# Optimization experiments

Measured on AMD Instinct MI355X. Metric: run time of the kernel, lower is better.

The kernel has to match this reference:

```python
import jax, jax.numpy as jnp
import numpy as np
from jax import lax

EPS = 1e-12

V, D, L, B = 50000, 128, 2048, 64
K1, K2 = 64, 64
W1, W2, W3 = 8, 8, 8


def conv1d_same(x, w):
    # x: [B, L, Cin], w: [W, Cin, Cout] -> [B, L, Cout]
    return lax.conv_general_dilated(x, w, window_strides=(1,), padding='SAME',
                                    dimension_numbers=('NWC', 'WIO', 'NWC'))


def gru_final_state(x, Wx, Wh, b):
    # Keras GRU (reset_after=True, gate order z, r, h); returns final hidden state.
    # x: [B, L, D] -> h_T: [B, K2]
    U = Wh.shape[0]
    x_proj = jnp.einsum('bld,dk->blk', x, Wx) + b[0]  # [B, L, 3U]

    def step(h, xp_t):
        hp = h @ Wh + b[1]                       # [B, 3U]
        xz, xr, xh = jnp.split(xp_t, 3, axis=-1)
        hz, hr, hh_ = jnp.split(hp, 3, axis=-1)
        z = jax.nn.sigmoid(xz + hz)
        r = jax.nn.sigmoid(xr + hr)
        hh = jnp.tanh(xh + r * hh_)
        h_new = z * h + (1.0 - z) * hh
        return h_new, None

    h0 = jnp.zeros((x.shape[0], U), dtype=x.dtype)
    h_T, _ = lax.scan(step, h0, jnp.swapaxes(x_proj, 0, 1))
    return h_T


def setup_inputs() -> dict:
    key = jax.random.key(0)
    ks = jax.random.split(key, 10)
    s = 0.05
    return {
        'code_block': jax.random.randint(ks[0], (B, L), 0, V, dtype=jnp.int32),
        'E': jax.random.normal(ks[1], (V, D), jnp.float32) * s,
        'bias_table': jax.random.normal(ks[2], (V, 1), jnp.float32) * s,
        'Wx': jax.random.normal(ks[3], (D, 3 * K2), jnp.float32) * s,
        'Wh': jax.random.normal(ks[4], (K2, 3 * K2), jnp.float32) * s,
        'b_gru': jnp.zeros((2, 3 * K2), jnp.float32),
        'c1w': jax.random.normal(ks[5], (W1, D, K1), jnp.float32) * s,
        'c1b': jnp.zeros((K1,), jnp.float32),
        'c2w': jax.random.normal(ks[6], (W2, K1, K2), jnp.float32) * s,
        'c2b': jnp.zeros((K2,), jnp.float32),
        'c3w': jax.random.normal(ks[7], (W3, K2, 1), jnp.float32) * s,
        'c3b': jnp.zeros((1,), jnp.float32),
    }


def reference(code_block, E, bias_table, Wx, Wh, b_gru, c1w, c1b, c2w, c2b, c3w, c3b):
    tok = E[code_block]                          # [B, L, D] embedding gather
    bias = bias_table[code_block][..., 0]        # [B, L] per-token bias

    h_t = gru_final_state(tok, Wx, Wh, b_gru)    # [B, K2]

    # AttentionFeatures: conv -> relu -> conv -> * h_t -> l2-normalize (dropout off)
    L1 = jax.nn.relu(conv1d_same(tok, c1w) + c1b)        # [B, L, K1]
    L2 = (conv1d_same(L1, c2w) + c2b) * h_t[:, None, :]  # [B, L, K2]
    L_feat = L2 * lax.rsqrt(jnp.sum(L2 * L2, axis=-1, keepdims=True) + EPS)

    # AttentionWeights: conv to 1 channel, softmax over time
    a_logits = conv1d_same(L_feat, c3w)[..., 0] + c3b    # [B, L]
    alpha = jax.nn.softmax(a_logits, axis=-1)            # [B, L]

    # n_hat = sum_l alpha_l * embed_l
    n_hat = jnp.einsum('bl,bld->bd', alpha, tok)         # [B, D]

    # logits_l = <embed_l, n_hat> + bias_l ; softmax over positions
    logits = jnp.einsum('bld,bd->bl', tok, n_hat) + bias # [B, L]
    return jax.nn.softmax(logits, axis=-1)
```

## Files before the change

### kernel.cpp

```cpp
#include <hip/hip_runtime.h>

#define B_ 64
#define L_ 2048
#define D_ 128
#define LP 2056
#define PAD 3

typedef __attribute__((ext_vector_type(8))) short short8;
typedef __attribute__((ext_vector_type(4))) float f32x4;
typedef __attribute__((ext_vector_type(4))) unsigned short us4;

static __device__ __forceinline__ float bf2f(unsigned short u) {
  return __uint_as_float(((unsigned int)u) << 16);
}
static __device__ __forceinline__ unsigned short f2bf(float f) {
  unsigned int x = __float_as_uint(f);
  unsigned int r = (x + 0x7fffu + ((x >> 16) & 1u)) >> 16;
  return (unsigned short)r;
}

__global__ __launch_bounds__(256) void k_prep(
    const int* __restrict__ code, const float* __restrict__ E,
    const float* __restrict__ bias_table, const float* __restrict__ Wx,
    const float* __restrict__ c1w, const float* __restrict__ c2w,
    unsigned short* __restrict__ tokpad,
    unsigned short* __restrict__ WxT, unsigned short* __restrict__ c1wT,
    unsigned short* __restrict__ c2wT, float* __restrict__ biasg)
{
  int id = blockIdx.x * 256 + threadIdx.x;
  const int N0 = B_ * LP * 16;
  if (id < N0) {
    int b = id / (LP * 16); int rem = id % (LP * 16);
    int row = rem >> 4, c8 = rem & 15;
    uint4 o = {0u,0u,0u,0u};
    if (row >= PAD && row < PAD + L_) {
      int cd = code[b * L_ + (row - PAD)];
      const float4* e = (const float4*)(E + (size_t)cd * D_ + c8 * 8);
      float4 e0 = e[0], e1 = e[1];
      o.x = f2bf(e0.x) | ((unsigned int)f2bf(e0.y) << 16);
      o.y = f2bf(e0.z) | ((unsigned int)f2bf(e0.w) << 16);
      o.z = f2bf(e1.x) | ((unsigned int)f2bf(e1.y) << 16);
      o.w = f2bf(e1.z) | ((unsigned int)f2bf(e1.w) << 16);
    }
    ((uint4*)tokpad)[id] = o;
    return;
  }
  id -= N0;
  const int N2 = B_ * L_;
  if (id < N2) { biasg[id] = bias_table[code[id]]; return; }
  id -= N2;
  const int N3 = 192 * 128;
  if (id < N3) { int c = id >> 7, d = id & 127; WxT[id] = f2bf(Wx[d * 192 + c]); return; }
  id -= N3;
  const int N4 = 8 * 64 * 128;
  if (id < N4) {
    int w = id >> 13, c = (id >> 7) & 63, d = id & 127;
    c1wT[id] = f2bf(c1w[(w * 128 + d) * 64 + c]); return;
  }
  id -= N4;
  const int N5 = 8 * 64 * 64;
  if (id < N5) {
    int w = id >> 12, c = (id >> 6) & 63, d = id & 63;
    c2wT[id] = f2bf(c2w[(w * 64 + d) * 64 + c]);
  }
}

__global__ __launch_bounds__(256) void k_xproj(
    const unsigned short* __restrict__ tokpad, const unsigned short* __restrict__ WxT,
    const float* __restrict__ bg, unsigned short* __restrict__ xg)
{
  __shared__ __align__(16) unsigned short At[128 * 136];
  __shared__ __align__(16) unsigned short Bt[192 * 136];
  int b = blockIdx.x >> 4;
  int l0 = (blockIdx.x & 15) << 7;
  int tid = threadIdx.x;
  for (int i = tid; i < 128 * 16; i += 256) {
    int row = i >> 4, c8 = i & 15;
    uint4 v = ((const uint4*)tokpad)[(b * LP + PAD + l0 + row) * 16 + c8];
    *((uint4*)&At[row * 136 + c8 * 8]) = v;
  }
  for (int i = tid; i < 192 * 16; i += 256) {
    int row = i >> 4, c8 = i & 15;
    uint4 v = ((const uint4*)WxT)[i];
    *((uint4*)&Bt[row * 136 + c8 * 8]) = v;
  }
  __syncthreads();
  int wave = tid >> 6, lane = tid & 63;
  int m = lane & 15, q = lane >> 4;
  f32x4 acc[2][12];
  #pragma unroll
  for (int mt = 0; mt < 2; ++mt)
    #pragma unroll
    for (int nt = 0; nt < 12; ++nt) acc[mt][nt] = (f32x4){0.f,0.f,0.f,0.f};
  #pragma unroll
  for (int ks = 0; ks < 4; ++ks) {
    int kof = ks * 32 + q * 8;
    short8 a[2], bb[12];
    #pragma unroll
    for (int mt = 0; mt < 2; ++mt)
      a[mt] = *(const short8*)&At[(wave * 32 + mt * 16 + m) * 136 + kof];
    #pragma unroll
    for (int nt = 0; nt < 12; ++nt)
      bb[nt] = *(const short8*)&Bt[(nt * 16 + m) * 136 + kof];
    #pragma unroll
    for (int mt = 0; mt < 2; ++mt)
      #pragma unroll
      for (int nt = 0; nt < 12; ++nt)
        acc[mt][nt] = __builtin_amdgcn_mfma_f32_16x16x32_bf16(a[mt], bb[nt], acc[mt][nt], 0, 0, 0);
  }
  __syncthreads();
  #pragma unroll
  for (int mt = 0; mt < 2; ++mt) {
    int lrow = wave * 32 + mt * 16 + q * 4;
    #pragma unroll
    for (int nt = 0; nt < 12; ++nt) {
      int c = nt * 16 + m;
      float b0 = bg[c];
      us4 val;
      val.x = f2bf(acc[mt][nt][0] + b0);
      val.y = f2bf(acc[mt][nt][1] + b0);
      val.z = f2bf(acc[mt][nt][2] + b0);
      val.w = f2bf(acc[mt][nt][3] + b0);
      *((us4*)&Bt[c * 136 + lrow]) = val;
    }
  }
  __syncthreads();
  for (int i = tid; i < 64 * 32; i += 256) {
    int j = i >> 5, g = i & 31;
    us4 z4 = *(const us4*)&Bt[j * 136 + g * 4];
    us4 r4 = *(const us4*)&Bt[(64 + j) * 136 + g * 4];
    us4 h4 = *(const us4*)&Bt[(128 + j) * 136 + g * 4];
    uint4 o0, o1;
    o0.x = (unsigned)z4.x | ((unsigned)r4.x << 16); o0.y = (unsigned)h4.x;
    o0.z = (unsigned)z4.y | ((unsigned)r4.y << 16); o0.w = (unsigned)h4.y;
    o1.x = (unsigned)z4.z | ((unsigned)r4.z << 16); o1.y = (unsigned)h4.z;
    o1.z = (unsigned)z4.w | ((unsigned)r4.w << 16); o1.w = (unsigned)h4.w;
    size_t stp = (size_t)(b * 64 + j) * L_ + l0 + g * 4;
    ((uint4*)xg)[stp >> 1]       = o0;
    ((uint4*)xg)[(stp >> 1) + 1] = o1;
  }
}

#define BARRIER() asm volatile("s_waitcnt lgkmcnt(0)\n\ts_barrier" ::: "memory")

__global__ __launch_bounds__(192)
__attribute__((amdgpu_waves_per_eu(1, 1)))
void k_fused(
    const unsigned short* __restrict__ xg, const float* __restrict__ Wh,
    const float* __restrict__ bg, float* __restrict__ h_t,
    const unsigned short* __restrict__ tokpad,
    const unsigned short* __restrict__ c1wT, const float* __restrict__ c1b,
    const unsigned short* __restrict__ c2wT, const float* __restrict__ c2b,
    unsigned short* __restrict__ c2o)
{
  __shared__ __align__(16) unsigned short pool[39744];
  int bid = blockIdx.x;
  int tid = threadIdx.x;

  if (bid < 64) {
    int w = tid >> 6, j = tid & 63;
    float* xch = (float*)pool;
    int b = bid;
    int kb = w * 22;

    float wz[22], wr[22], wh[22];
    #pragma unroll
    for (int i = 0; i < 22; ++i) {
      int k = kb + i;
      bool ok = k < 64;
      wz[i] = ok ? Wh[k * 192 + j]       : 0.f;
      wr[i] = ok ? Wh[k * 192 + 64 + j]  : 0.f;
      wh[i] = ok ? Wh[k * 192 + 128 + j] : 0.f;
    }
    #pragma unroll
    for (int i = 0; i < 22; ++i)
      asm volatile("" : "+v"(wz[i]), "+v"(wr[i]), "+v"(wh[i]));

    float seedz = (w == 0) ? bg[192 + j]       : 0.f;
    float seedr = (w == 0) ? bg[192 + 64 + j]  : 0.f;
    float seedh = (w == 0) ? bg[192 + 128 + j] : 0.f;
    float hreg = 0.f;

    const uint4* xp = (const uint4*)(xg + (size_t)(b * 64 + j) * L_ * 4);
    uint4 cur_ = xp[0];
    uint4 nxt_ = xp[1];

#define STEP(WZR, WH_, P) { \
    float hk[22]; \
    _Pragma("unroll") \
    for (int i = 0; i < 22; ++i) \
      hk[i] = __int_as_float(__builtin_amdgcn_readlane(__float_as_int(hreg), (kb + i) & 63)); \
    __builtin_amdgcn_sched_barrier(0); \
    float az[4] = {seedz, 0.f, 0.f, 0.f}; \
    float ar[4] = {seedr, 0.f, 0.f, 0.f}; \
    float ah[4] = {seedh, 0.f, 0.f, 0.f}; \
    _Pragma("unroll") \
    for (int i = 0; i < 22; ++i) { \
      az[i & 3] = fmaf(hk[i], wz[i], az[i & 3]); \
      ar[i & 3] = fmaf(hk[i], wr[i], ar[i & 3]); \
      ah[i & 3] = fmaf(hk[i], wh[i], ah[i & 3]); \
    } \
    float4 pv; \
    pv.x = (az[0] + az[1]) + (az[2] + az[3]); \
    pv.y = (ar[0] + ar[1]) + (ar[2] + ar[3]); \
    pv.z = (ah[0] + ah[1]) + (ah[2] + ah[3]); \
    pv.w = 0.f; \
    *((float4*)&xch[(P) * 768 + (w * 64 + j) * 4]) = pv; \
    BARRIER(); \
    float4 q0 = *((const float4*)&xch[(P) * 768 + (0 * 64 + j) * 4]); \
    float4 q1 = *((const float4*)&xch[(P) * 768 + (1 * 64 + j) * 4]); \
    float4 q2 = *((const float4*)&xch[(P) * 768 + (2 * 64 + j) * 4]); \
    float sz = (q0.x + q1.x) + q2.x; \
    float sr = (q0.y + q1.y) + q2.y; \
    float sh = (q0.z + q1.z) + q2.z; \
    float xvz = bf2f((unsigned short)((WZR) & 0xffffu)); \
    float xvr = bf2f((unsigned short)((WZR) >> 16)); \
    float xvh = bf2f((unsigned short)((WH_) & 0xffffu)); \
    float zg = 1.f / (1.f + __expf(-(xvz + sz))); \
    float rg = 1.f / (1.f + __expf(-(xvr + sr))); \
    float e2 = __expf(-2.f * (xvh + rg * sh)); \
    float hh = fmaf(2.f, __frcp_rn(1.f + e2), -1.f); \
    hreg = zg * hreg + (1.f - zg) * hh; \
  }

    #pragma nounroll
    for (int p = 0; p < L_ / 2; ++p) {
      int pn = (p < L_ / 2 - 2) ? p + 2 : (L_ / 2 - 1);
      uint4 nn = xp[pn];
      STEP(cur_.x, cur_.y, 0)
      STEP(cur_.z, cur_.w, 1)
      cur_ = nxt_; nxt_ = nn;
    }
#undef STEP
    if (w == 0) h_t[b * 64 + j] = hreg;
    return;
  }

  unsigned short* At    = pool;
  unsigned short* l1buf = pool + 20672;
  unsigned short* Bw    = pool + 31040;
  int wv = tid >> 6, lane = tid & 63;
  int m = lane & 15, q = lane >> 4;

  for (int job = bid - 64; job < 1024; job += 192) {
    int b = job >> 4;
    int l0 = (job & 15) << 7;
    __syncthreads();
    for (int i = tid; i < 152 * 16; i += 192) {
      int row = i >> 4, c8 = i & 15;
      int p = l0 - 3 + row;
      p = p < 0 ? 0 : (p > 2055 ? 2055 : p);
      *((uint4*)&At[row * 136 + c8 * 8]) = ((const uint4*)tokpad)[(b * LP + p) * 16 + c8];
    }
    f32x4 acc[3][4];
    #pragma unroll
    for (int mt = 0; mt < 3; ++mt)
      #pragma unroll
      for (int nt = 0; nt < 4; ++nt) acc[mt][nt] = (f32x4){0.f,0.f,0.f,0.f};
    for (int w8 = 0; w8 < 8; ++w8) {
      __syncthreads();
      for (int i = tid; i < 64 * 16; i += 192) {
        int row = i >> 4, c8 = i & 15;
        *((uint4*)&Bw[row * 136 + c8 * 8]) = ((const uint4*)c1wT)[(w8 * 64 + row) * 16 + c8];
      }
      __syncthreads();
      #pragma unroll
      for (int ks = 0; ks < 4; ++ks) {
        int kof = ks * 32 + q * 8;
        short8 a[3], bb[4];
        #pragma unroll
        for (int mt = 0; mt < 3; ++mt) {
          int tl = wv + 3 * mt;
          a[mt] = *(const short8*)&At[(tl * 16 + m + w8) * 136 + kof];
        }
        #pragma unroll
        for (int nt = 0; nt < 4; ++nt)
          bb[nt] = *(const short8*)&Bw[(nt * 16 + m) * 136 + kof];
        #pragma unroll
        for (int mt = 0; mt < 3; ++mt)
          #pragma unroll
          for (int nt = 0; nt < 4; ++nt)
            acc[mt][nt] = __builtin_amdgcn_mfma_f32_16x16x32_bf16(a[mt], bb[nt], acc[mt][nt], 0, 0, 0);
      }
    }
    #pragma unroll
    for (int mt = 0; mt < 3; ++mt) {
      int tl = wv + 3 * mt;
      #pragma unroll
      for (int nt = 0; nt < 4; ++nt) {
        int c = nt * 16 + m;
        float bs = c1b[c];
        #pragma unroll
        for (int r = 0; r < 4; ++r) {
          float v = fmaxf(acc[mt][nt][r] + bs, 0.f);
          l1buf[(tl * 16 + q * 4 + r) * 72 + c] = f2bf(v);
        }
      }
    }
    __syncthreads();
    for (int i2 = tid; i2 < 135 * 8; i2 += 192) {
      int i = i2 >> 3, c8 = i2 & 7;
      int jrow = l0 - 3 + i;
      if (jrow < 0 || jrow > 2047) {
        uint4 z4 = {0u,0u,0u,0u};
        *((uint4*)&l1buf[i * 72 + c8 * 8]) = z4;
      }
    }
    f32x4 acc2[3][4];
    #pragma unroll
    for (int mt = 0; mt < 3; ++mt)
      #pragma unroll
      for (int nt = 0; nt < 4; ++nt) acc2[mt][nt] = (f32x4){0.f,0.f,0.f,0.f};
    for (int w8 = 0; w8 < 8; ++w8) {
      __syncthreads();
      for (int i = tid; i < 64 * 8; i += 192) {
        int row = i >> 3, c8 = i & 7;
        *((uint4*)&Bw[row * 72 + c8 * 8]) = ((const uint4*)c2wT)[(w8 * 64 + row) * 8 + c8];
      }
      __syncthreads();
      #pragma unroll
      for (int ks = 0; ks < 2; ++ks) {
        int kof = ks * 32 + q * 8;
        short8 a[3], bb[4];
        #pragma unroll
        for (int mt = 0; mt < 3; ++mt) {
          int tl = wv + 3 * mt;
          if (tl < 8)
            a[mt] = *(const short8*)&l1buf[(tl * 16 + m + w8) * 72 + kof];
        }
        #pragma unroll
        for (int nt = 0; nt < 4; ++nt)
          bb[nt] = *(const short8*)&Bw[(nt * 16 + m) * 72 + kof];
        #pragma unroll
        for (int mt = 0; mt < 3; ++mt) {
          int tl = wv + 3 * mt;
          if (tl < 8)
            #pragma unroll
            for (int nt = 0; nt < 4; ++nt)
              acc2[mt][nt] = __builtin_amdgcn_mfma_f32_16x16x32_bf16(a[mt], bb[nt], acc2[mt][nt], 0, 0, 0);
        }
      }
    }
    #pragma unroll
    for (int mt = 0; mt < 3; ++mt) {
      int tl = wv + 3 * mt;
      if (tl < 8) {
        #pragma unroll
        for (int nt = 0; nt < 4; ++nt) {
          int c = nt * 16 + m;
          float bs = c2b[c];
          #pragma unroll
          for (int r = 0; r < 4; ++r)
            c2o[(size_t)(b * L_ + l0 + tl * 16 + q * 4 + r) * 64 + c] = f2bf(acc2[mt][nt][r] + bs);
        }
      }
    }
  }
}

__global__ __launch_bounds__(256) void k_alpha(
    const unsigned short* __restrict__ c2o, const float* __restrict__ h_t,
    const float* __restrict__ c3w, const float* __restrict__ c3b,
    float* __restrict__ a_out)
{
  __shared__ float Lf[71 * 65];
  __shared__ float red[256];
  __shared__ float ht[64];
  __shared__ float c3[512];
  int b = blockIdx.x >> 5;
  int tile = blockIdx.x & 31;
  int tid = threadIdx.x, lane = tid & 63, wave = tid >> 6;
  if (tid < 64) ht[tid] = h_t[b * 64 + tid];
  for (int i = tid; i < 512; i += 256) c3[i] = c3w[i];
  float c3bias = c3b[0];
  __syncthreads();
  int lt = tile << 6;
  for (int i0 = wave; i0 < 71; i0 += 4) {
    int l = lt - 3 + i0;
    float v = 0.f;
    if (l >= 0 && l < L_) v = bf2f(c2o[((size_t)b * L_ + l) * 64 + lane]) * ht[lane];
    float ss = v * v;
    #pragma unroll
    for (int msk = 1; msk < 64; msk <<= 1) ss += __shfl_xor(ss, msk);
    Lf[i0 * 65 + lane] = v * rsqrtf(ss + 1e-12f);
  }
  __syncthreads();
  {
    int u = lane, part = wave;
    float p = 0.f;
    #pragma unroll
    for (int w = 0; w < 8; ++w)
      #pragma unroll
      for (int cc = 0; cc < 16; ++cc) {
        int c = part * 16 + cc;
        p += Lf[(u + w) * 65 + c] * c3[w * 64 + c];
      }
    red[tid] = p;
  }
  __syncthreads();
  if (tid < 64)
    a_out[b * L_ + lt + tid] = red[tid] + red[64 + tid] + red[128 + tid] + red[192 + tid] + c3bias;
}

__global__ __launch_bounds__(256) void k_fin(
    const unsigned short* __restrict__ tokpad, const float* __restrict__ a_in,
    const float* __restrict__ biasg, float* __restrict__ out)
{
  __shared__ float a_lds[2048];
  __shared__ float l_lds[2048];
  __shared__ float red[256];
  __shared__ float nred[512];
  __shared__ float nhat[128];
  int b = blockIdx.x, tid = threadIdx.x, lane = tid & 63, wave = tid >> 6;
  for (int i = tid; i < 2048; i += 256) a_lds[i] = a_in[b * L_ + i];
  __syncthreads();
  {
    float mx = -1e30f;
    for (int i = tid; i < 2048; i += 256) mx = fmaxf(mx, a_lds[i]);
    #pragma unroll
    for (int msk = 1; msk < 64; msk <<= 1) mx = fmaxf(mx, __shfl_xor(mx, msk));
    if (lane == 0) red[wave] = mx;
    __syncthreads();
    mx = fmaxf(fmaxf(red[0], red[1]), fmaxf(red[2], red[3]));
    float sm = 0.f;
    for (int i = tid; i < 2048; i += 256) sm += __expf(a_lds[i] - mx);
    #pragma unroll
    for (int msk = 1; msk < 64; msk <<= 1) sm += __shfl_xor(sm, msk);
    __syncthreads();
    if (lane == 0) red[wave] = sm;
    __syncthreads();
    sm = red[0] + red[1] + red[2] + red[3];
    float inv = 1.f / sm;
    for (int i = tid; i < 2048; i += 256) a_lds[i] = __expf(a_lds[i] - mx) * inv;
    __syncthreads();
  }
  {
    int d2 = tid & 63, g = tid >> 6;
    float ax = 0.f, ay = 0.f;
    for (int l = g; l < L_; l += 4) {
      unsigned int uu = *(const unsigned int*)&tokpad[((size_t)b * LP + PAD + l) * 128 + d2 * 2];
      float al = a_lds[l];
      ax += al * bf2f((unsigned short)(uu & 0xffffu));
      ay += al * bf2f((unsigned short)(uu >> 16));
    }
    nred[g * 128 + d2 * 2] = ax;
    nred[g * 128 + d2 * 2 + 1] = ay;
    __syncthreads();
    if (tid < 128) nhat[tid] = nred[tid] + nred[128 + tid] + nred[256 + tid] + nred[384 + tid];
    __syncthreads();
  }
  for (int li = 0; li < 8; ++li) {
    int l = li * 256 + tid;
    const uint4* rowp = (const uint4*)&tokpad[((size_t)b * LP + PAD + l) * 128];
    float s = 0.f;
    #pragma unroll
    for (int jj = 0; jj < 16; ++jj) {
      uint4 uu = rowp[jj];
      s += bf2f((unsigned short)(uu.x & 0xffffu)) * nhat[jj*8+0]
         + bf2f((unsigned short)(uu.x >> 16))     * nhat[jj*8+1]
         + bf2f((unsigned short)(uu.y & 0xffffu)) * nhat[jj*8+2]
         + bf2f((unsigned short)(uu.y >> 16))     * nhat[jj*8+3]
         + bf2f((unsigned short)(uu.z & 0xffffu)) * nhat[jj*8+4]
         + bf2f((unsigned short)(uu.z >> 16))     * nhat[jj*8+5]
         + bf2f((unsigned short)(uu.w & 0xffffu)) * nhat[jj*8+6]
         + bf2f((unsigned short)(uu.w >> 16))     * nhat[jj*8+7];
    }
    l_lds[l] = s + biasg[b * L_ + l];
  }
  __syncthreads();
  {
    float mx = -1e30f;
    for (int i = tid; i < 2048; i += 256) mx = fmaxf(mx, l_lds[i]);
    #pragma unroll
    for (int msk = 1; msk < 64; msk <<= 1) mx = fmaxf(mx, __shfl_xor(mx, msk));
    __syncthreads();
    if (lane == 0) red[wave] = mx;
    __syncthreads();
    mx = fmaxf(fmaxf(red[0], red[1]), fmaxf(red[2], red[3]));
    float sm = 0.f;
    for (int i = tid; i < 2048; i += 256) sm += __expf(l_lds[i] - mx);
    #pragma unroll
    for (int msk = 1; msk < 64; msk <<= 1) sm += __shfl_xor(sm, msk);
    __syncthreads();
    if (lane == 0) red[wave] = sm;
    __syncthreads();
    sm = red[0] + red[1] + red[2] + red[3];
    float inv = 1.f / sm;
    for (int i = tid; i < 2048; i += 256) out[b * L_ + i] = __expf(l_lds[i] - mx) * inv;
  }
}

extern "C" void kernel_launch(void* const* d_in, const int* in_sizes, int n_in,
                              void* d_out, int out_size, void* d_ws, size_t ws_size,
                              hipStream_t stream) {
  const int*   code = (const int*)d_in[0];
  const float* E    = (const float*)d_in[1];
  const float* bt   = (const float*)d_in[2];
  const float* Wx   = (const float*)d_in[3];
  const float* Wh   = (const float*)d_in[4];
  const float* bg   = (const float*)d_in[5];
  const float* c1w  = (const float*)d_in[6];
  const float* c1b  = (const float*)d_in[7];
  const float* c2w  = (const float*)d_in[8];
  const float* c2b  = (const float*)d_in[9];
  const float* c3w  = (const float*)d_in[10];
  const float* c3b  = (const float*)d_in[11];
  char* ws = (char*)d_ws;
  unsigned short* tokpad = (unsigned short*)(ws);
  unsigned short* xg     = (unsigned short*)(ws + 33685504);
  unsigned short* c2o    = (unsigned short*)(ws + 100794368);
  unsigned short* WxT    = (unsigned short*)(ws + 117571584);
  unsigned short* c1wT   = (unsigned short*)(ws + 117620736);
  unsigned short* c2wT   = (unsigned short*)(ws + 117751808);
  float*          htp    = (float*)(ws + 117817344);
  float*          biasg  = (float*)(ws + 117833728);
  float*          alog   = (float*)(ws + 33685504);

  k_prep <<<9216, 256, 0, stream>>>(code, E, bt, Wx, c1w, c2w, tokpad, WxT, c1wT, c2wT, biasg);
  k_xproj<<<1024, 256, 0, stream>>>(tokpad, WxT, bg, xg);
  k_fused<<<256, 192, 0, stream>>>(xg, Wh, bg, htp, tokpad, c1wT, c1b, c2wT, c2b, c2o);
  k_alpha<<<2048, 256, 0, stream>>>(c2o, htp, c3w, c3b, alog);
  k_fin  <<<64, 256, 0, stream>>>(tokpad, alog, biasg, (float*)d_out);
}
```

Before: 1.219 ms.

## Split final softmax/attention kernel into four kernels with wider grids

The single 64-block final kernel is split into softmax-over-alpha, a 512-block partial n_hat reduction, a 512-block logits kernel and a final softmax kernel. The two tokpad passes then run across many more CUs instead of one block per batch row. This adds three kernel launches and round-trips alpha, partial sums and logits through global memory.

Result: faster. 1.079 ms (-11.5%).

```diff
diff --git a/kernel.cpp b/kernel.cpp
--- a/kernel.cpp
+++ b/kernel.cpp
@@ -402,92 +402,113 @@
     a_out[b * L_ + lt + tid] = red[tid] + red[64 + tid] + red[128 + tid] + red[192 + tid] + c3bias;
 }
 
-__global__ __launch_bounds__(256) void k_fin(
-    const unsigned short* __restrict__ tokpad, const float* __restrict__ a_in,
-    const float* __restrict__ biasg, float* __restrict__ out)
+__global__ __launch_bounds__(256) void k_soft1(float* __restrict__ a)
 {
   __shared__ float a_lds[2048];
+  __shared__ float red[256];
+  int b = blockIdx.x, tid = threadIdx.x, lane = tid & 63, wave = tid >> 6;
+  for (int i = tid; i < 2048; i += 256) a_lds[i] = a[b * L_ + i];
+  __syncthreads();
+  float mx = -1e30f;
+  for (int i = tid; i < 2048; i += 256) mx = fmaxf(mx, a_lds[i]);
+  #pragma unroll
+  for (int msk = 1; msk < 64; msk <<= 1) mx = fmaxf(mx, __shfl_xor(mx, msk));
+  if (lane == 0) red[wave] = mx;
+  __syncthreads();
+  mx = fmaxf(fmaxf(red[0], red[1]), fmaxf(red[2], red[3]));
+  float sm = 0.f;
+  for (int i = tid; i < 2048; i += 256) sm += __expf(a_lds[i] - mx);
+  #pragma unroll
+  for (int msk = 1; msk < 64; msk <<= 1) sm += __shfl_xor(sm, msk);
+  __syncthreads();
+  if (lane == 0) red[wave] = sm;
+  __syncthreads();
+  sm = red[0] + red[1] + red[2] + red[3];
+  float inv = 1.f / sm;
+  for (int i = tid; i < 2048; i += 256) a[b * L_ + i] = __expf(a_lds[i] - mx) * inv;
+}
+
+__global__ __launch_bounds__(256) void k_nhat(
+    const unsigned short* __restrict__ tokpad, const float* __restrict__ alpha,
+    float* __restrict__ npart)
+{
+  __shared__ float nred[512];
+  int b = blockIdx.x >> 3, c = blockIdx.x & 7;
+  int tid = threadIdx.x;
+  int d2 = tid & 63, g = tid >> 6;
+  int l0 = c << 8;
+  float ax = 0.f, ay = 0.f;
+  for (int i = 0; i < 64; ++i) {
+    int l = l0 + g + 4 * i;
+    unsigned int uu = *(const unsigned int*)&tokpad[((size_t)b * LP + PAD + l) * 128 + d2 * 2];
+    float al = alpha[b * L_ + l];
+    ax += al * bf2f((unsigned short)(uu & 0xffffu));
+    ay += al * bf2f((unsigned short)(uu >> 16));
+  }
+  nred[g * 128 + d2 * 2] = ax;
+  nred[g * 128 + d2 * 2 + 1] = ay;
+  __syncthreads();
+  if (tid < 128)
+    npart[((b << 3) + c) * 128 + tid] = nred[tid] + nred[128 + tid] + nred[256 + tid] + nred[384 + tid];
+}
+
+__global__ __launch_bounds__(256) void k_logits(
+    const unsigned short* __restrict__ tokpad, const float* __restrict__ npart,
+    const float* __restrict__ biasg, float* __restrict__ l_all)
+{
+  __shared__ float nhat[128];
+  int b = blockIdx.x >> 3, c = blockIdx.x & 7;
+  int tid = threadIdx.x;
+  if (tid < 128) {
+    const float* p = npart + (b << 3) * 128 + tid;
+    nhat[tid] = ((p[0] + p[128]) + (p[256] + p[384]))
+              + ((p[512] + p[640]) + (p[768] + p[896]));
+  }
+  __syncthreads();
+  int l = (c << 8) + tid;
+  const uint4* rowp = (const uint4*)&tokpad[((size_t)b * LP + PAD + l) * 128];
+  float s = 0.f;
+  #pragma unroll
+  for (int jj = 0; jj < 16; ++jj) {
+    uint4 uu = rowp[jj];
+    s += bf2f((unsigned short)(uu.x & 0xffffu)) * nhat[jj*8+0]
+       + bf2f((unsigned short)(uu.x >> 16))     * nhat[jj*8+1]
+       + bf2f((unsigned short)(uu.y & 0xffffu)) * nhat[jj*8+2]
+       + bf2f((unsigned short)(uu.y >> 16))     * nhat[jj*8+3]
+       + bf2f((unsigned short)(uu.z & 0xffffu)) * nhat[jj*8+4]
+       + bf2f((unsigned short)(uu.z >> 16))     * nhat[jj*8+5]
+       + bf2f((unsigned short)(uu.w & 0xffffu)) * nhat[jj*8+6]
+       + bf2f((unsigned short)(uu.w >> 16))     * nhat[jj*8+7];
+  }
+  l_all[b * L_ + l] = s + biasg[b * L_ + l];
+}
+
+__global__ __launch_bounds__(256) void k_soft2(
+    const float* __restrict__ l_all, float* __restrict__ out)
+{
   __shared__ float l_lds[2048];
   __shared__ float red[256];
-  __shared__ float nred[512];
-  __shared__ float nhat[128];
   int b = blockIdx.x, tid = threadIdx.x, lane = tid & 63, wave = tid >> 6;
-  for (int i = tid; i < 2048; i += 256) a_lds[i] = a_in[b * L_ + i];
-  __syncthreads();
-  {
-    float mx = -1e30f;
-    for (int i = tid; i < 2048; i += 256) mx = fmaxf(mx, a_lds[i]);
-    #pragma unroll
-    for (int msk = 1; msk < 64; msk <<= 1) mx = fmaxf(mx, __shfl_xor(mx, msk));
-    if (lane == 0) red[wave] = mx;
-    __syncthreads();
-    mx = fmaxf(fmaxf(red[0], red[1]), fmaxf(red[2], red[3]));
-    float sm = 0.f;
-    for (int i = tid; i < 2048; i += 256) sm += __expf(a_lds[i] - mx);
-    #pragma unroll
-    for (int msk = 1; msk < 64; msk <<= 1) sm += __shfl_xor(sm, msk);
-    __syncthreads();
-    if (lane == 0) red[wave] = sm;
-    __syncthreads();
-    sm = red[0] + red[1] + red[2] + red[3];
-    float inv = 1.f / sm;
-    for (int i = tid; i < 2048; i += 256) a_lds[i] = __expf(a_lds[i] - mx) * inv;
-    __syncthreads();
-  }
-  {
-    int d2 = tid & 63, g = tid >> 6;
-    float ax = 0.f, ay = 0.f;
-    for (int l = g; l < L_; l += 4) {
-      unsigned int uu = *(const unsigned int*)&tokpad[((size_t)b * LP + PAD + l) * 128 + d2 * 2];
-      float al = a_lds[l];
-      ax += al * bf2f((unsigned short)(uu & 0xffffu));
-      ay += al * bf2f((unsigned short)(uu >> 16));
-    }
-    nred[g * 128 + d2 * 2] = ax;
-    nred[g * 128 + d2 * 2 + 1] = ay;
-    __syncthreads();
-    if (tid < 128) nhat[tid] = nred[tid] + nred[128 + tid] + nred[256 + tid] + nred[384 + tid];
-    __syncthreads();
-  }
-  for (int li = 0; li < 8; ++li) {
-    int l = li * 256 + tid;
-    const uint4* rowp = (const uint4*)&tokpad[((size_t)b * LP + PAD + l) * 128];
-    float s = 0.f;
-    #pragma unroll
-    for (int jj = 0; jj < 16; ++jj) {
-      uint4 uu = rowp[jj];
-      s += bf2f((unsigned short)(uu.x & 0xffffu)) * nhat[jj*8+0]
-         + bf2f((unsigned short)(uu.x >> 16))     * nhat[jj*8+1]
-         + bf2f((unsigned short)(uu.y & 0xffffu)) * nhat[jj*8+2]
-         + bf2f((unsigned short)(uu.y >> 16))     * nhat[jj*8+3]
-         + bf2f((unsigned short)(uu.z & 0xffffu)) * nhat[jj*8+4]
-         + bf2f((unsigned short)(uu.z >> 16))     * nhat[jj*8+5]
-         + bf2f((unsigned short)(uu.w & 0xffffu)) * nhat[jj*8+6]
-         + bf2f((unsigned short)(uu.w >> 16))     * nhat[jj*8+7];
-    }
-    l_lds[l] = s + biasg[b * L_ + l];
-  }
-  __syncthreads();
-  {
-    float mx = -1e30f;
-    for (int i = tid; i < 2048; i += 256) mx = fmaxf(mx, l_lds[i]);
-    #pragma unroll
-    for (int msk = 1; msk < 64; msk <<= 1) mx = fmaxf(mx, __shfl_xor(mx, msk));
-    __syncthreads();
-    if (lane == 0) red[wave] = mx;
-    __syncthreads();
-    mx = fmaxf(fmaxf(red[0], red[1]), fmaxf(red[2], red[3]));
-    float sm = 0.f;
-    for (int i = tid; i < 2048; i += 256) sm += __expf(l_lds[i] - mx);
-    #pragma unroll
-    for (int msk = 1; msk < 64; msk <<= 1) sm += __shfl_xor(sm, msk);
-    __syncthreads();
-    if (lane == 0) red[wave] = sm;
-    __syncthreads();
-    sm = red[0] + red[1] + red[2] + red[3];
-    float inv = 1.f / sm;
-    for (int i = tid; i < 2048; i += 256) out[b * L_ + i] = __expf(l_lds[i] - mx) * inv;
-  }
+  for (int i = tid; i < 2048; i += 256) l_lds[i] = l_all[b * L_ + i];
+  __syncthreads();
+  float mx = -1e30f;
+  for (int i = tid; i < 2048; i += 256) mx = fmaxf(mx, l_lds[i]);
+  #pragma unroll
+  for (int msk = 1; msk < 64; msk <<= 1) mx = fmaxf(mx, __shfl_xor(mx, msk));
+  __syncthreads();
+  if (lane == 0) red[wave] = mx;
+  __syncthreads();
+  mx = fmaxf(fmaxf(red[0], red[1]), fmaxf(red[2], red[3]));
+  float sm = 0.f;
+  for (int i = tid; i < 2048; i += 256) sm += __expf(l_lds[i] - mx);
+  #pragma unroll
+  for (int msk = 1; msk < 64; msk <<= 1) sm += __shfl_xor(sm, msk);
+  __syncthreads();
+  if (lane == 0) red[wave] = sm;
+  __syncthreads();
+  sm = red[0] + red[1] + red[2] + red[3];
+  float inv = 1.f / sm;
+  for (int i = tid; i < 2048; i += 256) out[b * L_ + i] = __expf(l_lds[i] - mx) * inv;
 }
 
 extern "C" void kernel_launch(void* const* d_in, const int* in_sizes, int n_in,
@@ -515,10 +536,15 @@
   float*          htp    = (float*)(ws + 117817344);
   float*          biasg  = (float*)(ws + 117833728);
   float*          alog   = (float*)(ws + 33685504);
-
-  k_prep <<<9216, 256, 0, stream>>>(code, E, bt, Wx, c1w, c2w, tokpad, WxT, c1wT, c2wT, biasg);
-  k_xproj<<<1024, 256, 0, stream>>>(tokpad, WxT, bg, xg);
-  k_fused<<<256, 192, 0, stream>>>(xg, Wh, bg, htp, tokpad, c1wT, c1b, c2wT, c2b, c2o);
-  k_alpha<<<2048, 256, 0, stream>>>(c2o, htp, c3w, c3b, alog);
-  k_fin  <<<64, 256, 0, stream>>>(tokpad, alog, biasg, (float*)d_out);
-}
+  float*          npart  = (float*)(ws + 33685504 + 1048576);
+  float*          l_all  = (float*)(ws + 33685504 + 2097152);
+
+  k_prep  <<<9216, 256, 0, stream>>>(code, E, bt, Wx, c1w, c2w, tokpad, WxT, c1wT, c2wT, biasg);
+  k_xproj <<<1024, 256, 0, stream>>>(tokpad, WxT, bg, xg);
+  k_fused <<<256, 192, 0, stream>>>(xg, Wh, bg, htp, tokpad, c1wT, c1b, c2wT, c2b, c2o);
+  k_alpha <<<2048, 256, 0, stream>>>(c2o, htp, c3w, c3b, alog);
+  k_soft1 <<<64, 256, 0, stream>>>(alog);
+  k_nhat  <<<512, 256, 0, stream>>>(tokpad, alog, npart);
+  k_logits<<<512, 256, 0, stream>>>(tokpad, npart, biasg, l_all);
+  k_soft2 <<<64, 256, 0, stream>>>(l_all, (float*)d_out);
+}
```
